# Kernel tuning notes

Measured on AMD Instinct MI355X. Metric: run time of the kernel, lower is better.

The kernel has to match this reference:

```python
import jax, jax.numpy as jnp
import numpy as np

N = 50000   # total nodes in batch
E = 640000  # directed edges
G = 64      # graphs in batch
D_IN = 128
D_H = 128
D_OUT = 10


def _glorot(key, shape):
    fan_in = shape[0]
    return jax.random.normal(key, shape, dtype=jnp.float32) / np.sqrt(fan_in)


def setup_inputs() -> dict:
    key = jax.random.key(0)
    ks = jax.random.split(key, 10)
    x = jax.random.normal(ks[0], (N, D_IN), dtype=jnp.float32)
    src = jax.random.randint(ks[1], (E,), 0, N, dtype=jnp.int32)
    dst = jax.random.randint(ks[2], (E,), 0, N, dtype=jnp.int32)
    batch = jnp.sort(jax.random.randint(ks[3], (N,), 0, G, dtype=jnp.int32))
    return {
        "x": x, "src": src, "dst": dst, "batch": batch,
        "W1": _glorot(ks[4], (D_IN, D_H)), "b1": jnp.zeros((D_H,), jnp.float32),
        "W2": _glorot(ks[5], (D_H, D_H)), "b2": jnp.zeros((D_H,), jnp.float32),
        "W3": _glorot(ks[6], (D_H, D_H)), "b3": jnp.zeros((D_H,), jnp.float32),
        "Wl": _glorot(ks[7], (D_H, D_OUT)), "bl": jnp.zeros((D_OUT,), jnp.float32),
    }


def gcn_conv(x, W, b, src, dst):
    """PyG GCNConv: add self-loops, symmetric deg^-1/2 normalization,
    linear transform, scatter-sum aggregation at dst, plus bias."""
    n = x.shape[0]
    loops = jnp.arange(n, dtype=src.dtype)
    s = jnp.concatenate([src, loops])  # [E+N]
    d = jnp.concatenate([dst, loops])
    deg = jax.ops.segment_sum(jnp.ones_like(d, dtype=x.dtype), d, num_segments=n)
    dinv = jnp.where(deg > 0, jax.lax.rsqrt(deg), 0.0)
    norm = dinv[s] * dinv[d]                        # [E+N]
    h = x @ W                                       # [N, D]
    out = jax.ops.segment_sum(h[s] * norm[:, None], d, num_segments=n)
    return out + b


def reference(x, src, dst, batch, W1, b1, W2, b2, W3, b3, Wl, bl):
    n = x.shape[0]
    h = jax.nn.relu(gcn_conv(x, W1, b1, src, dst))
    # dropout is a no-op in eval mode
    h = jax.nn.relu(gcn_conv(h, W2, b2, src, dst))
    h = gcn_conv(h, W3, b3, src, dst)
    # global_mean_pool over graph ids
    sums = jax.ops.segment_sum(h, batch, num_segments=G)            # [G, D]
    counts = jax.ops.segment_sum(jnp.ones((n,), h.dtype), batch, num_segments=G)
    pooled = sums / jnp.maximum(counts, 1.0)[:, None]
    logits = pooled @ Wl + bl                                       # [G, D_OUT]
    return jax.nn.log_softmax(logits, axis=1)
```

## Files before the change

kernel.cpp:

```cpp
#include <hip/hip_runtime.h>


constexpr int D = 128;
constexpr int DOUT = 10;
constexpr int PSPLIT = 8;
constexpr int BSH = 3;
constexpr int BCAP = 192;
constexpr int CPAD = 16;

using short8  = __attribute__((ext_vector_type(8))) short;
using float4v = __attribute__((ext_vector_type(4))) float;
using f32x2   = __attribute__((ext_vector_type(2))) float;

__device__ __forceinline__ ushort f2bf(float f) {
  uint u = __float_as_uint(f);
  return (ushort)((u + 0x7fffu + ((u >> 16) & 1u)) >> 16);
}
__device__ __forceinline__ float bf2f(ushort s) {
  return __uint_as_float(((uint)s) << 16);
}
__device__ __forceinline__ float bfhi(uint u) { return __uint_as_float(u & 0xffff0000u); }


__global__ void init_kernel(int* __restrict__ bcnt, int total) {
  int i = blockIdx.x * blockDim.x + threadIdx.x;
  if (i < total) bcnt[i] = 0;
}

__global__ void binfill_kernel(const int* __restrict__ src, const int* __restrict__ dst,
    int* __restrict__ bcnt, uint* __restrict__ buck, int e) {
  int i = blockIdx.x * blockDim.x + threadIdx.x;
  if (i >= e) return;
  int d = dst[i], s = src[i];
  int b = d >> BSH;
  int pos = atomicAdd(&bcnt[b * CPAD], 1);
  if (pos < BCAP)
    buck[(size_t)b * BCAP + pos] = (uint)s | ((uint)(d & ((1 << BSH) - 1)) << 16);
}

__global__ __launch_bounds__(256) void countb_kernel(const uint* __restrict__ buck,
    const int* __restrict__ bcnt, int* __restrict__ cnt, int n) {
  __shared__ int lc[256];
  const int base = blockIdx.x * 256;
  const int m = min(256, n - base);
  for (int j = threadIdx.x; j < m; j += 256) lc[j] = 0;
  __syncthreads();
  const int b0 = base >> BSH;
  #pragma unroll
  for (int bb = 0; bb < (256 >> BSH); ++bb) {
    int b = b0 + bb;
    if ((b << BSH) >= n) break;
    int c = min(bcnt[b * CPAD], BCAP);
    for (int i = threadIdx.x; i < c; i += 256)
      atomicAdd(&lc[(bb << BSH) + (int)(buck[(size_t)b * BCAP + i] >> 16)], 1);
  }
  __syncthreads();
  for (int j = threadIdx.x; j < m; j += 256) cnt[base + j] = lc[j];
}

__global__ __launch_bounds__(256) void scan1_kernel(const int* __restrict__ cnt,
    int* __restrict__ bsum, int n) {
  __shared__ int sd[256];
  int i = blockIdx.x * 256 + threadIdx.x;
  sd[threadIdx.x] = (i < n) ? cnt[i] : 0;
  __syncthreads();
  for (int off = 128; off > 0; off >>= 1) {
    if (threadIdx.x < (unsigned)off) sd[threadIdx.x] += sd[threadIdx.x + off];
    __syncthreads();
  }
  if (threadIdx.x == 0) bsum[blockIdx.x] = sd[0];
}

__global__ __launch_bounds__(1024) void scan2_kernel(const int* __restrict__ bsum,
    int* __restrict__ boff, int nb, int* __restrict__ rowptr, int n) {
  __shared__ int sd[1024];
  int v = ((int)threadIdx.x < nb) ? bsum[threadIdx.x] : 0;
  sd[threadIdx.x] = v;
  __syncthreads();
  for (int off = 1; off < 1024; off <<= 1) {
    int t = (threadIdx.x >= (unsigned)off) ? sd[threadIdx.x - off] : 0;
    __syncthreads();
    sd[threadIdx.x] += t;
    __syncthreads();
  }
  if ((int)threadIdx.x < nb) boff[threadIdx.x] = sd[threadIdx.x] - v;
  if ((int)threadIdx.x == nb - 1) rowptr[n] = sd[threadIdx.x];
}

__global__ __launch_bounds__(256) void scan3_kernel(const int* __restrict__ cnt,
    const int* __restrict__ boff, int* __restrict__ rowptr,
    float* __restrict__ dinv, int n) {
  __shared__ int sd[256];
  int i = blockIdx.x * 256 + threadIdx.x;
  int v = (i < n) ? cnt[i] : 0;
  sd[threadIdx.x] = v;
  __syncthreads();
  for (int off = 1; off < 256; off <<= 1) {
    int t = (threadIdx.x >= (unsigned)off) ? sd[threadIdx.x - off] : 0;
    __syncthreads();
    sd[threadIdx.x] += t;
    __syncthreads();
  }
  if (i < n) {
    rowptr[i] = boff[blockIdx.x] + sd[threadIdx.x] - v;
    dinv[i] = rsqrtf((float)(v + 1));
  }
}

__global__ __launch_bounds__(256) void scatter_kernel(const uint* __restrict__ buck,
    const int* __restrict__ bcnt, const int* __restrict__ rowptr,
    const float* __restrict__ dinv, uint* __restrict__ epk, int n) {
  __shared__ int lcur[256];
  const int base = blockIdx.x * 256;
  const int m = min(256, n - base);
  for (int j = threadIdx.x; j < m; j += 256) lcur[j] = rowptr[base + j];
  __syncthreads();
  const int b0 = base >> BSH;
  #pragma unroll
  for (int bb = 0; bb < (256 >> BSH); ++bb) {
    int b = b0 + bb;
    if ((b << BSH) >= n) break;
    int c = min(bcnt[b * CPAD], BCAP);
    for (int i = threadIdx.x; i < c; i += 256) {
      uint rec = buck[(size_t)b * BCAP + i];
      int dl = (int)(rec >> 16);
      int s = (int)(rec & 0xffffu);
      int d = (b << BSH) + dl;
      int slot = atomicAdd(&lcur[(bb << BSH) + dl], 1);
      epk[slot] = (uint)s | ((uint)f2bf(dinv[s] * dinv[d]) << 16);
    }
  }
}

__global__ __launch_bounds__(256) void prepw_kernel(const float* __restrict__ W1,
    const float* __restrict__ W2, const float* __restrict__ W3, ushort* __restrict__ Wp) {
  const float* W = (blockIdx.y == 0) ? W1 : (blockIdx.y == 1) ? W2 : W3;
  ushort* Wpo = Wp + (size_t)blockIdx.y * 2048 * 8;
  int idx = blockIdx.x * 256 + threadIdx.x;
  int cf = idx >> 8, kk = (idx >> 6) & 3, lane = idx & 63;
  int k0 = kk * 32 + (lane >> 4) * 8;
  int c = cf * 16 + (lane & 15);
  uint p[4];
  #pragma unroll
  for (int h = 0; h < 4; ++h) {
    ushort lo = f2bf(W[(k0 + 2 * h) * D + c]);
    ushort hi = f2bf(W[(k0 + 2 * h + 1) * D + c]);
    p[h] = (uint)lo | ((uint)hi << 16);
  }
  uint4 w = make_uint4(p[0], p[1], p[2], p[3]);
  *(uint4*)(Wpo + idx * 8) = w;
}

template<bool F32>
__global__ __launch_bounds__(256) void gemm_mfma(const void* __restrict__ Ain,
    const ushort* __restrict__ Wp, uchar* __restrict__ out, int n) {
  __shared__ ushort wl[2048 * 8];
  const int tid = threadIdx.x;
  #pragma unroll
  for (int i = 0; i < 8; ++i) {
    int idx = tid + i * 256;
    *(uint4*)(&wl[idx * 8]) = *(const uint4*)(Wp + idx * 8);
  }
  __syncthreads();
  const int w = tid >> 6, lane = tid & 63;
  const int row0 = blockIdx.x * 64 + w * 16;
  int arow = row0 + (lane & 15);
  if (arow >= n) arow = n - 1;

  short8 a[4];
  if constexpr (F32) {
    const float* abase = (const float*)Ain + (size_t)arow * D + ((lane >> 4) * 8);
    #pragma unroll
    for (int kk = 0; kk < 4; ++kk) {
      float4 f0 = *(const float4*)(abase + kk * 32);
      float4 f1 = *(const float4*)(abase + kk * 32 + 4);
      short8 v;
      v[0] = (short)f2bf(f0.x); v[1] = (short)f2bf(f0.y);
      v[2] = (short)f2bf(f0.z); v[3] = (short)f2bf(f0.w);
      v[4] = (short)f2bf(f1.x); v[5] = (short)f2bf(f1.y);
      v[6] = (short)f2bf(f1.z); v[7] = (short)f2bf(f1.w);
      a[kk] = v;
    }
  } else {
    const ushort* abase = (const ushort*)Ain + (size_t)arow * D + ((lane >> 4) * 8);
    #pragma unroll
    for (int kk = 0; kk < 4; ++kk) a[kk] = *(const short8*)(abase + kk * 32);
  }

  float4v acc[8] = {};
  #pragma unroll
  for (int kk = 0; kk < 4; ++kk) {
    #pragma unroll
    for (int cf = 0; cf < 8; ++cf) {
      short8 b = *(const short8*)(&wl[((cf * 4 + kk) * 64 + lane) * 8]);
      acc[cf] = __builtin_amdgcn_mfma_f32_16x16x32_bf16(a[kk], b, acc[cf], 0, 0, 0);
    }
  }
  const int crow = row0 + (lane >> 4) * 4;
  const int ccol = lane & 15;
  #pragma unroll
  for (int cf = 0; cf < 8; ++cf) {
    #pragma unroll
    for (int r = 0; r < 4; ++r) {
      if (crow + r < n) {
        int enc = __builtin_amdgcn_cvt_pk_fp8_f32(acc[cf][r], acc[cf][r], 0, false);
        out[(size_t)(crow + r) * D + cf * 16 + ccol] = (uchar)(enc & 0xff);
      }
    }
  }
}

__global__ __launch_bounds__(256) void agg_kernel(const uchar* __restrict__ h8,
    const int* __restrict__ rowptr, const uint* __restrict__ epk,
    const float* __restrict__ dinv, const float* __restrict__ bias,
    ushort* __restrict__ out, int n, int relu) {
  int node = (int)((blockIdx.x * blockDim.x + threadIdx.x) >> 6);
  if (node >= n) return;
  const int lane = threadIdx.x & 63;
  const int sub = lane >> 5;
  const int li = lane & 31;
  const int beg = rowptr[node], end = rowptr[node + 1];
  float a0 = 0.f, a1 = 0.f, a2 = 0.f, a3 = 0.f;
  for (int e = beg; e < end; e += 8) {
    int i0 = e + 0 + sub, i1 = e + 2 + sub, i2 = e + 4 + sub, i3 = e + 6 + sub;
    uint m0 = epk[min(i0, end - 1)];
    uint m1 = epk[min(i1, end - 1)];
    uint m2 = epk[min(i2, end - 1)];
    uint m3 = epk[min(i3, end - 1)];
    uint r0 = *(const uint*)(h8 + (size_t)(m0 & 0xffffu) * D + li * 4);
    uint r1 = *(const uint*)(h8 + (size_t)(m1 & 0xffffu) * D + li * 4);
    uint r2 = *(const uint*)(h8 + (size_t)(m2 & 0xffffu) * D + li * 4);
    uint r3 = *(const uint*)(h8 + (size_t)(m3 & 0xffffu) * D + li * 4);
    float w0 = (i0 < end) ? bfhi(m0) : 0.f;
    float w1 = (i1 < end) ? bfhi(m1) : 0.f;
    float w2 = (i2 < end) ? bfhi(m2) : 0.f;
    float w3 = (i3 < end) ? bfhi(m3) : 0.f;
    f32x2 p0a = __builtin_amdgcn_cvt_pk_f32_fp8(r0, false);
    f32x2 p0b = __builtin_amdgcn_cvt_pk_f32_fp8(r0, true);
    f32x2 p1a = __builtin_amdgcn_cvt_pk_f32_fp8(r1, false);
    f32x2 p1b = __builtin_amdgcn_cvt_pk_f32_fp8(r1, true);
    f32x2 p2a = __builtin_amdgcn_cvt_pk_f32_fp8(r2, false);
    f32x2 p2b = __builtin_amdgcn_cvt_pk_f32_fp8(r2, true);
    f32x2 p3a = __builtin_amdgcn_cvt_pk_f32_fp8(r3, false);
    f32x2 p3b = __builtin_amdgcn_cvt_pk_f32_fp8(r3, true);
    a0 += p0a[0] * w0 + p1a[0] * w1 + p2a[0] * w2 + p3a[0] * w3;
    a1 += p0a[1] * w0 + p1a[1] * w1 + p2a[1] * w2 + p3a[1] * w3;
    a2 += p0b[0] * w0 + p1b[0] * w1 + p2b[0] * w2 + p3b[0] * w3;
    a3 += p0b[1] * w0 + p1b[1] * w1 + p2b[1] * w2 + p3b[1] * w3;
  }
  a0 += __shfl_xor(a0, 32);
  a1 += __shfl_xor(a1, 32);
  a2 += __shfl_xor(a2, 32);
  a3 += __shfl_xor(a3, 32);
  const float di = dinv[node];
  const float dsq = di * di;
  uint sv = *(const uint*)(h8 + (size_t)node * D + li * 4);
  f32x2 sa = __builtin_amdgcn_cvt_pk_f32_fp8(sv, false);
  f32x2 sb = __builtin_amdgcn_cvt_pk_f32_fp8(sv, true);
  a0 += sa[0] * dsq;
  a1 += sa[1] * dsq;
  a2 += sb[0] * dsq;
  a3 += sb[1] * dsq;
  float4 bv = *(const float4*)(bias + li * 4);
  a0 += bv.x; a1 += bv.y; a2 += bv.z; a3 += bv.w;
  if (relu) {
    a0 = fmaxf(a0, 0.f); a1 = fmaxf(a1, 0.f);
    a2 = fmaxf(a2, 0.f); a3 = fmaxf(a3, 0.f);
  }
  if (sub == 0) {
    uint2 pk;
    pk.x = (uint)f2bf(a0) | ((uint)f2bf(a1) << 16);
    pk.y = (uint)f2bf(a2) | ((uint)f2bf(a3) << 16);
    *(uint2*)(out + (size_t)node * D + li * 4) = pk;
  }
}

__global__ __launch_bounds__(256) void pool1_kernel(const ushort* __restrict__ act,
    const int* __restrict__ batch, float* __restrict__ pp, int n) {
  const int g = blockIdx.x;
  const int sp = blockIdx.y;
  int lo = 0, hi = n;
  while (lo < hi) { int mid = (lo + hi) >> 1; if (batch[mid] < g) lo = mid + 1; else hi = mid; }
  const int start = lo;
  hi = n;
  while (lo < hi) { int mid = (lo + hi) >> 1; if (batch[mid] <= g) lo = mid + 1; else hi = mid; }
  const int end = lo;
  const int len = end - start;
  const int per = (len + PSPLIT - 1) / PSPLIT;
  const int i0 = start + sp * per;
  const int i1 = min(i0 + per, end);

  const int rt = threadIdx.x >> 4;
  const int ds = threadIdx.x & 15;
  float acc[8] = {};
  for (int i = i0 + rt; i < i1; i += 16) {
    short8 v = *(const short8*)(act + (size_t)i * D + ds * 8);
    #pragma unroll
    for (int e2 = 0; e2 < 8; ++e2) acc[e2] += bf2f((ushort)v[e2]);
  }
  __shared__ float sd[256][8];
  #pragma unroll
  for (int e2 = 0; e2 < 8; ++e2) sd[threadIdx.x][e2] = acc[e2];
  __syncthreads();
  if (threadIdx.x < 128) {
    int d = threadIdx.x;
    int slice = d >> 3, e2 = d & 7;
    float s = 0.f;
    #pragma unroll
    for (int k = 0; k < 16; ++k) s += sd[k * 16 + slice][e2];
    pp[((size_t)g * PSPLIT + sp) * D + d] = s;
  }
}

__global__ __launch_bounds__(640) void head_kernel(const float* __restrict__ pp,
    const int* __restrict__ batch, const float* __restrict__ Wl,
    const float* __restrict__ bl, float* __restrict__ out, int n, int g) {
  __shared__ float pooled[64 * D];
  __shared__ float cnts[64];
  __shared__ float lg[64][DOUT];
  const int tid = threadIdx.x;
  if (tid < g) {
    int gg = tid;
    int lo = 0, hi = n;
    while (lo < hi) { int mid = (lo + hi) >> 1; if (batch[mid] < gg) lo = mid + 1; else hi = mid; }
    int start = lo;
    hi = n;
    while (lo < hi) { int mid = (lo + hi) >> 1; if (batch[mid] <= gg) lo = mid + 1; else hi = mid; }
    cnts[gg] = fmaxf((float)(lo - start), 1.f);
  }
  __syncthreads();
  for (int idx = tid; idx < g * D; idx += 640) {
    int gg = idx >> 7, d = idx & 127;
    float s = 0.f;
    #pragma unroll
    for (int sp = 0; sp < PSPLIT; ++sp) s += pp[((size_t)gg * PSPLIT + sp) * D + d];
    pooled[idx] = s / cnts[gg];
  }
  __syncthreads();
  int gi = tid / DOUT, o = tid % DOUT;
  if (gi < g) {
    float acc = bl[o];
    for (int d = 0; d < D; ++d) acc += pooled[gi * D + d] * Wl[d * DOUT + o];
    lg[gi][o] = acc;
  }
  __syncthreads();
  if (gi < g) {
    float m = -1e30f;
    for (int j = 0; j < DOUT; ++j) m = fmaxf(m, lg[gi][j]);
    float s = 0.f;
    for (int j = 0; j < DOUT; ++j) s += expf(lg[gi][j] - m);
    out[gi * DOUT + o] = lg[gi][o] - m - logf(s);
  }
}


extern "C" void kernel_launch(void* const* d_in, const int* in_sizes, int n_in,
                              void* d_out, int out_size, void* d_ws, size_t ws_size,
                              hipStream_t stream) {
  const float* x   = (const float*)d_in[0];
  const int* src   = (const int*)d_in[1];
  const int* dst   = (const int*)d_in[2];
  const int* batch = (const int*)d_in[3];
  const float* W1  = (const float*)d_in[4];
  const float* b1  = (const float*)d_in[5];
  const float* W2  = (const float*)d_in[6];
  const float* b2  = (const float*)d_in[7];
  const float* W3  = (const float*)d_in[8];
  const float* b3  = (const float*)d_in[9];
  const float* Wl  = (const float*)d_in[10];
  const float* bl  = (const float*)d_in[11];
  float* out = (float*)d_out;

  const int n = in_sizes[0] / D;
  const int e = in_sizes[1];
  const int g = out_size / DOUT;

  char* p = (char*)d_ws;
  auto alloc = [&](size_t bytes) {
    char* r = p;
    p += (bytes + 255) & ~(size_t)255;
    return r;
  };
  const int nb = (n + 255) / 256;
  const int NB = (n + (1 << BSH) - 1) >> BSH;
  const int NGRP = (n + 255) / 256;
  int* cnt      = (int*)alloc((size_t)n * 4);
  int* rowptr   = (int*)alloc((size_t)(n + 1) * 4);
  float* dinv   = (float*)alloc((size_t)n * 4);
  int* bsum     = (int*)alloc((size_t)nb * 4);
  int* boff     = (int*)alloc((size_t)nb * 4);
  int* bcnt     = (int*)alloc((size_t)NB * CPAD * 4);
  uint* buck    = (uint*)alloc((size_t)NB * BCAP * 4);
  uint* epk     = (uint*)alloc((size_t)e * 4);
  ushort* Wp    = (ushort*)alloc(3 * 2048 * 16);
  ushort* bfA   = (ushort*)alloc((size_t)n * D * 2);
  ushort* bfB   = (ushort*)alloc((size_t)n * D * 2);
  uchar* tmp8   = (uchar*)alloc((size_t)n * D);
  float* pp     = (float*)alloc((size_t)g * PSPLIT * D * 4);
  (void)ws_size;

  const int B = 256;
  const int gridE = (e + B - 1) / B;

  init_kernel<<<(NB * CPAD + B - 1) / B, B, 0, stream>>>(bcnt, NB * CPAD);
  binfill_kernel<<<gridE, B, 0, stream>>>(src, dst, bcnt, buck, e);
  countb_kernel<<<NGRP, B, 0, stream>>>(buck, bcnt, cnt, n);
  scan1_kernel<<<nb, B, 0, stream>>>(cnt, bsum, n);
  scan2_kernel<<<1, 1024, 0, stream>>>(bsum, boff, nb, rowptr, n);
  scan3_kernel<<<nb, B, 0, stream>>>(cnt, boff, rowptr, dinv, n);
  scatter_kernel<<<NGRP, B, 0, stream>>>(buck, bcnt, rowptr, dinv, epk, n);
  prepw_kernel<<<dim3(8, 3), B, 0, stream>>>(W1, W2, W3, Wp);

  const int gemmGrid = (n + 63) / 64;
  const int aggGrid = (n * 64 + B - 1) / B;

  gemm_mfma<true><<<gemmGrid, B, 0, stream>>>(x, Wp, tmp8, n);
  agg_kernel<<<aggGrid, B, 0, stream>>>(tmp8, rowptr, epk, dinv, b1, bfB, n, 1);
  gemm_mfma<false><<<gemmGrid, B, 0, stream>>>(bfB, Wp + 2048 * 8, tmp8, n);
  agg_kernel<<<aggGrid, B, 0, stream>>>(tmp8, rowptr, epk, dinv, b2, bfA, n, 1);
  gemm_mfma<false><<<gemmGrid, B, 0, stream>>>(bfA, Wp + 2 * 2048 * 8, tmp8, n);
  agg_kernel<<<aggGrid, B, 0, stream>>>(tmp8, rowptr, epk, dinv, b3, bfB, n, 0);

  pool1_kernel<<<dim3(g, PSPLIT), B, 0, stream>>>(bfB, batch, pp, n);
  head_kernel<<<1, 640, 0, stream>>>(pp, batch, Wl, bl, out, n, g);
}
```

Measured before the change: 211.1 us.

## Fuse CSR build scan stages into count/scatter kernels and unroll aggregation deeper

Merges the block-sum scan into the bucket count kernel and the final scan plus dinv computation into count/scatter, which removes two kernel launches and the cnt/rowptr round trips. Separately, the aggregation loop now processes 16 edges per iteration with 8 independent gathers per half-wave to raise memory-level parallelism. The trade-offs are more registers per thread in agg and more wasted clamped loads for low-degree nodes.

```diff
diff --git a/kernel.cpp b/kernel.cpp
--- a/kernel.cpp
+++ b/kernel.cpp
@@ -39,11 +39,12 @@
 }
 
 __global__ __launch_bounds__(256) void countb_kernel(const uint* __restrict__ buck,
-    const int* __restrict__ bcnt, int* __restrict__ cnt, int n) {
+    const int* __restrict__ bcnt, int* __restrict__ cnt, float* __restrict__ dinv,
+    int* __restrict__ bsum, int n) {
   __shared__ int lc[256];
   const int base = blockIdx.x * 256;
   const int m = min(256, n - base);
-  for (int j = threadIdx.x; j < m; j += 256) lc[j] = 0;
+  lc[threadIdx.x] = 0;
   __syncthreads();
   const int b0 = base >> BSH;
   #pragma unroll
@@ -55,14 +56,13 @@
       atomicAdd(&lc[(bb << BSH) + (int)(buck[(size_t)b * BCAP + i] >> 16)], 1);
   }
   __syncthreads();
-  for (int j = threadIdx.x; j < m; j += 256) cnt[base + j] = lc[j];
-}
-
-__global__ __launch_bounds__(256) void scan1_kernel(const int* __restrict__ cnt,
-    int* __restrict__ bsum, int n) {
+  int v = lc[threadIdx.x];
+  if ((int)threadIdx.x < m) {
+    cnt[base + threadIdx.x] = v;
+    dinv[base + threadIdx.x] = rsqrtf((float)(v + 1));
+  }
   __shared__ int sd[256];
-  int i = blockIdx.x * 256 + threadIdx.x;
-  sd[threadIdx.x] = (i < n) ? cnt[i] : 0;
+  sd[threadIdx.x] = ((int)threadIdx.x < m) ? v : 0;
   __syncthreads();
   for (int off = 128; off > 0; off >>= 1) {
     if (threadIdx.x < (unsigned)off) sd[threadIdx.x] += sd[threadIdx.x + off];
@@ -87,11 +87,15 @@
   if ((int)threadIdx.x == nb - 1) rowptr[n] = sd[threadIdx.x];
 }
 
-__global__ __launch_bounds__(256) void scan3_kernel(const int* __restrict__ cnt,
+__global__ __launch_bounds__(256) void scatter_kernel(const uint* __restrict__ buck,
+    const int* __restrict__ bcnt, const int* __restrict__ cnt,
     const int* __restrict__ boff, int* __restrict__ rowptr,
-    float* __restrict__ dinv, int n) {
+    const float* __restrict__ dinv, uint* __restrict__ epk, int n) {
   __shared__ int sd[256];
-  int i = blockIdx.x * 256 + threadIdx.x;
+  __shared__ int lcur[256];
+  const int base = blockIdx.x * 256;
+  const int m = min(256, n - base);
+  const int i = base + (int)threadIdx.x;
   int v = (i < n) ? cnt[i] : 0;
   sd[threadIdx.x] = v;
   __syncthreads();
@@ -101,19 +105,11 @@
     sd[threadIdx.x] += t;
     __syncthreads();
   }
+  int rp = boff[blockIdx.x] + sd[threadIdx.x] - v;
   if (i < n) {
-    rowptr[i] = boff[blockIdx.x] + sd[threadIdx.x] - v;
-    dinv[i] = rsqrtf((float)(v + 1));
-  }
-}
-
-__global__ __launch_bounds__(256) void scatter_kernel(const uint* __restrict__ buck,
-    const int* __restrict__ bcnt, const int* __restrict__ rowptr,
-    const float* __restrict__ dinv, uint* __restrict__ epk, int n) {
-  __shared__ int lcur[256];
-  const int base = blockIdx.x * 256;
-  const int m = min(256, n - base);
-  for (int j = threadIdx.x; j < m; j += 256) lcur[j] = rowptr[base + j];
+    rowptr[i] = rp;
+    lcur[threadIdx.x] = rp;
+  }
   __syncthreads();
   const int b0 = base >> BSH;
   #pragma unroll
@@ -121,8 +117,8 @@
     int b = b0 + bb;
     if ((b << BSH) >= n) break;
     int c = min(bcnt[b * CPAD], BCAP);
-    for (int i = threadIdx.x; i < c; i += 256) {
-      uint rec = buck[(size_t)b * BCAP + i];
+    for (int j = threadIdx.x; j < c; j += 256) {
+      uint rec = buck[(size_t)b * BCAP + j];
       int dl = (int)(rec >> 16);
       int s = (int)(rec & 0xffffu);
       int d = (b << BSH) + dl;
@@ -221,32 +217,24 @@
   const int li = lane & 31;
   const int beg = rowptr[node], end = rowptr[node + 1];
   float a0 = 0.f, a1 = 0.f, a2 = 0.f, a3 = 0.f;
-  for (int e = beg; e < end; e += 8) {
-    int i0 = e + 0 + sub, i1 = e + 2 + sub, i2 = e + 4 + sub, i3 = e + 6 + sub;
-    uint m0 = epk[min(i0, end - 1)];
-    uint m1 = epk[min(i1, end - 1)];
-    uint m2 = epk[min(i2, end - 1)];
-    uint m3 = epk[min(i3, end - 1)];
-    uint r0 = *(const uint*)(h8 + (size_t)(m0 & 0xffffu) * D + li * 4);
-    uint r1 = *(const uint*)(h8 + (size_t)(m1 & 0xffffu) * D + li * 4);
-    uint r2 = *(const uint*)(h8 + (size_t)(m2 & 0xffffu) * D + li * 4);
-    uint r3 = *(const uint*)(h8 + (size_t)(m3 & 0xffffu) * D + li * 4);
-    float w0 = (i0 < end) ? bfhi(m0) : 0.f;
-    float w1 = (i1 < end) ? bfhi(m1) : 0.f;
-    float w2 = (i2 < end) ? bfhi(m2) : 0.f;
-    float w3 = (i3 < end) ? bfhi(m3) : 0.f;
-    f32x2 p0a = __builtin_amdgcn_cvt_pk_f32_fp8(r0, false);
-    f32x2 p0b = __builtin_amdgcn_cvt_pk_f32_fp8(r0, true);
-    f32x2 p1a = __builtin_amdgcn_cvt_pk_f32_fp8(r1, false);
-    f32x2 p1b = __builtin_amdgcn_cvt_pk_f32_fp8(r1, true);
-    f32x2 p2a = __builtin_amdgcn_cvt_pk_f32_fp8(r2, false);
-    f32x2 p2b = __builtin_amdgcn_cvt_pk_f32_fp8(r2, true);
-    f32x2 p3a = __builtin_amdgcn_cvt_pk_f32_fp8(r3, false);
-    f32x2 p3b = __builtin_amdgcn_cvt_pk_f32_fp8(r3, true);
-    a0 += p0a[0] * w0 + p1a[0] * w1 + p2a[0] * w2 + p3a[0] * w3;
-    a1 += p0a[1] * w0 + p1a[1] * w1 + p2a[1] * w2 + p3a[1] * w3;
-    a2 += p0b[0] * w0 + p1b[0] * w1 + p2b[0] * w2 + p3b[0] * w3;
-    a3 += p0b[1] * w0 + p1b[1] * w1 + p2b[1] * w2 + p3b[1] * w3;
+  for (int e = beg; e < end; e += 16) {
+    uint mm[8], rr[8];
+    #pragma unroll
+    for (int k = 0; k < 8; ++k)
+      mm[k] = epk[min(e + 2 * k + sub, end - 1)];
+    #pragma unroll
+    for (int k = 0; k < 8; ++k)
+      rr[k] = *(const uint*)(h8 + (size_t)(mm[k] & 0xffffu) * D + li * 4);
+    #pragma unroll
+    for (int k = 0; k < 8; ++k) {
+      float wk = (e + 2 * k + sub < end) ? bfhi(mm[k]) : 0.f;
+      f32x2 pa = __builtin_amdgcn_cvt_pk_f32_fp8(rr[k], false);
+      f32x2 pb = __builtin_amdgcn_cvt_pk_f32_fp8(rr[k], true);
+      a0 += pa[0] * wk;
+      a1 += pa[1] * wk;
+      a2 += pb[0] * wk;
+      a3 += pb[1] * wk;
+    }
   }
   a0 += __shfl_xor(a0, 32);
   a1 += __shfl_xor(a1, 32);
@@ -383,7 +371,6 @@
   };
   const int nb = (n + 255) / 256;
   const int NB = (n + (1 << BSH) - 1) >> BSH;
-  const int NGRP = (n + 255) / 256;
   int* cnt      = (int*)alloc((size_t)n * 4);
   int* rowptr   = (int*)alloc((size_t)(n + 1) * 4);
   float* dinv   = (float*)alloc((size_t)n * 4);
@@ -404,11 +391,9 @@
 
   init_kernel<<<(NB * CPAD + B - 1) / B, B, 0, stream>>>(bcnt, NB * CPAD);
   binfill_kernel<<<gridE, B, 0, stream>>>(src, dst, bcnt, buck, e);
-  countb_kernel<<<NGRP, B, 0, stream>>>(buck, bcnt, cnt, n);
-  scan1_kernel<<<nb, B, 0, stream>>>(cnt, bsum, n);
+  countb_kernel<<<nb, B, 0, stream>>>(buck, bcnt, cnt, dinv, bsum, n);
   scan2_kernel<<<1, 1024, 0, stream>>>(bsum, boff, nb, rowptr, n);
-  scan3_kernel<<<nb, B, 0, stream>>>(cnt, boff, rowptr, dinv, n);
-  scatter_kernel<<<NGRP, B, 0, stream>>>(buck, bcnt, rowptr, dinv, epk, n);
+  scatter_kernel<<<nb, B, 0, stream>>>(buck, bcnt, cnt, boff, rowptr, dinv, epk, n);
   prepw_kernel<<<dim3(8, 3), B, 0, stream>>>(W1, W2, W3, Wp);
 
   const int gemmGrid = (n + 63) / 64;
```

Result: faster. 200.0 us (-5.2%).
